# Performance work log

Hardware: AMD Instinct MI355X
Metric: run time of the kernel (lower is better)

## Reference

```python
import jax, jax.numpy as jnp
import numpy as np

EPS = 1e-12  # TF l2_normalize epsilon


def setup_inputs() -> dict:
    key = jax.random.key(0)
    k1, k2 = jax.random.split(key)
    B, V, F = 32, 200000, 400000
    vertices = jax.random.normal(k1, (B, V, 3), dtype=jnp.float32)
    faces = jax.random.randint(k2, (F, 3), 0, V, dtype=jnp.int32)
    return {"vertices": vertices, "faces": faces}


def reference(vertices, faces):
    # vertices: [B, V, 3], faces: [F, 3]
    # Gather triangle vertices: [B, F, 3(verts), 3(xyz)]
    tri = vertices[:, faces, :]
    v0, v1, v2 = tri[..., 0, :], tri[..., 1, :], tri[..., 2, :]
    e1 = v0 - v1
    e2 = v2 - v1
    face_normals = jnp.cross(e2, e1)  # [B, F, 3], unnormalized
    # Scatter-add face normals onto each of the 3 face vertices
    vertex_normals = jnp.zeros_like(vertices)
    for i in range(3):
        vertex_normals = vertex_normals.at[:, faces[:, i], :].add(face_normals)
    # l2 normalize (TF semantics: x * rsqrt(max(sum(x^2), eps)))
    sq = jnp.sum(vertex_normals * vertex_normals, axis=-1, keepdims=True)
    vertex_normals = vertex_normals * jax.lax.rsqrt(jnp.maximum(sq, EPS))
    return vertex_normals
```

## Files before the change

### kernel.cpp

```cpp
#include <hip/hip_runtime.h>

#define EPS 1e-12f
#define CAP 32
#define CAPU 8

typedef unsigned long long ull;


__global__ void zero_ints(int* __restrict__ p, int n) {
    int i = blockIdx.x * blockDim.x + threadIdx.x;
    if (i < n) p[i] = 0;
}

__global__ __launch_bounds__(1024) void prep_kernel(const float* __restrict__ verts,
                                                    float* __restrict__ vT,
                                                    const int* __restrict__ faces,
                                                    int* __restrict__ cursor,
                                                    ull* __restrict__ ell,
                                                    int V, int tblk, int E) {
    if ((int)blockIdx.x < tblk) {
        __shared__ float sx[32][33], sy[32][33], sz[32][33];
        int tx = threadIdx.x & 31, ty = threadIdx.x >> 5;
        int v0 = blockIdx.x * 32;
        const float* p = verts + ((size_t)ty * V + (v0 + tx)) * 3;
        float x = __builtin_nontemporal_load(p + 0);
        float y = __builtin_nontemporal_load(p + 1);
        float z = __builtin_nontemporal_load(p + 2);
        sx[ty][tx] = x; sy[ty][tx] = y; sz[ty][tx] = z;
        __syncthreads();
        float* o = vT + (size_t)(v0 + ty) * 96;
        o[tx]      = sx[tx][ty];
        o[32 + tx] = sy[tx][ty];
        o[64 + tx] = sz[tx][ty];
    } else {
        int t = (blockIdx.x - tblk) * 1024 + threadIdx.x;
        if (t >= E) return;
        int f = t / 3;
        int c = t - 3 * f;
        int base = 3 * f;
        int iv = faces[base + c];
        int ia = faces[base + (c == 2 ? 0 : c + 1)];
        int ib = faces[base + (c == 0 ? 2 : c - 1)];
        int s = atomicAdd(&cursor[iv], 1);
        if (s < CAP) {
            ull e = ((ull)(unsigned)ib << 32) | (unsigned)ia;
            __builtin_nontemporal_store(e, ell + (size_t)iv * CAP + s);
        }
    }
}

__global__ __launch_bounds__(1024) void gather_t(const float* __restrict__ vT,
                                                 const int* __restrict__ deg,
                                                 const ull* __restrict__ ell,
                                                 float* __restrict__ out,
                                                 int V) {
    __shared__ float sx[32][33], sy[32][33], sz[32][33];
    int b = threadIdx.x & 31;
    int vi = threadIdx.x >> 5;
    int v = blockIdx.x * 32 + vi;

    int d = min(deg[v], CAP);
    const float* crow = vT + (size_t)v * 96;
    float vx = crow[b], vy = crow[32 + b], vz = crow[64 + b];
    const ull* ev = ell + (size_t)v * CAP;
    ull e[CAPU];
#pragma unroll
    for (int s = 0; s < CAPU; s++)
        e[s] = ev[s];
    __builtin_amdgcn_sched_barrier(0);

    float Ax[CAPU], Ay[CAPU], Az[CAPU], Bx[CAPU], By[CAPU], Bz[CAPU];
#pragma unroll
    for (int s = 0; s < CAPU; s++) {
        unsigned ia = (s < d) ? (unsigned)(e[s] & 0xffffffffull) : 0u;
        unsigned ib = (s < d) ? (unsigned)(e[s] >> 32) : 0u;
        const float* ra = vT + (size_t)ia * 96;
        const float* rb = vT + (size_t)ib * 96;
        Ax[s] = ra[b]; Ay[s] = ra[32 + b]; Az[s] = ra[64 + b];
        Bx[s] = rb[b]; By[s] = rb[32 + b]; Bz[s] = rb[64 + b];
    }
    __builtin_amdgcn_sched_barrier(0);

    float ax = 0.f, ay = 0.f, az = 0.f;
#pragma unroll
    for (int s = 0; s < CAPU; s++) {
        if (s < d) {
            float aX = Ax[s] - vx, aY = Ay[s] - vy, aZ = Az[s] - vz;
            float bX = Bx[s] - vx, bY = By[s] - vy, bZ = Bz[s] - vz;
            ax += aY * bZ - aZ * bY;
            ay += aZ * bX - aX * bZ;
            az += aX * bY - aY * bX;
        }
    }
    for (int s = CAPU; s < d; s++) {
        ull cu = ev[s];
        const float* ra = vT + (size_t)(unsigned)(cu & 0xffffffffull) * 96;
        const float* rb = vT + (size_t)(unsigned)(cu >> 32) * 96;
        float aX = ra[b] - vx, aY = ra[32 + b] - vy, aZ = ra[64 + b] - vz;
        float bX = rb[b] - vx, bY = rb[32 + b] - vy, bZ = rb[64 + b] - vz;
        ax += aY * bZ - aZ * bY;
        ay += aZ * bX - aX * bZ;
        az += aX * bY - aY * bX;
    }

    float scn = rsqrtf(fmaxf(ax * ax + ay * ay + az * az, EPS));
    sx[vi][b] = ax * scn; sy[vi][b] = ay * scn; sz[vi][b] = az * scn;
    __syncthreads();

    float* o = out + ((size_t)vi * V + (size_t)blockIdx.x * 32 + b) * 3;
    __builtin_nontemporal_store(sx[b][vi], o + 0);
    __builtin_nontemporal_store(sy[b][vi], o + 1);
    __builtin_nontemporal_store(sz[b][vi], o + 2);
}

extern "C" void kernel_launch(void* const* d_in, const int* in_sizes, int n_in,
                              void* d_out, int out_size, void* d_ws, size_t ws_size,
                              hipStream_t stream) {
    const float* verts = (const float*)d_in[0];
    const int* faces = (const int*)d_in[1];
    float* out = (float*)d_out;

    const int V = 200000;
    const int F = in_sizes[1] / 3;
    const int B = in_sizes[0] / (3 * V);
    const int E = 3 * F;
    (void)B;

    char* w = (char*)d_ws;
    float* vT = (float*)w;  w += (size_t)V * 96 * sizeof(float);
    int* cursor = (int*)w;  w += (size_t)V * sizeof(int);
    ull* ell = (ull*)w;

    zero_ints<<<(V + 255) / 256, 256, 0, stream>>>(cursor, V);

    int tblk = V / 32;
    int fblk = (E + 1023) / 1024;
    prep_kernel<<<tblk + fblk, 1024, 0, stream>>>(verts, vT, faces, cursor, ell,
                                                  V, tblk, E);

    gather_t<<<V / 32, 1024, 0, stream>>>(vT, cursor, ell, out, V);
}
```

Measured before the change: 398.6 us.

## Store corner indices instead of neighbor pairs and split prep into separate kernels

The adjacency list now stores a 4-byte corner index per incident face instead of an 8-byte packed neighbor pair. The gather kernel recovers the two other face vertices by reading the faces array again. The fused transpose/fill kernel is split into two separate launches. This halves the adjacency storage and the bytes written during the fill, at the cost of an extra dependent load level (cidx, then faces, then vT) in the gather and one more kernel launch.

```diff
diff --git a/kernel.cpp b/kernel.cpp
--- a/kernel.cpp
+++ b/kernel.cpp
@@ -12,46 +12,36 @@
     if (i < n) p[i] = 0;
 }
 
-__global__ __launch_bounds__(1024) void prep_kernel(const float* __restrict__ verts,
-                                                    float* __restrict__ vT,
-                                                    const int* __restrict__ faces,
-                                                    int* __restrict__ cursor,
-                                                    ull* __restrict__ ell,
-                                                    int V, int tblk, int E) {
-    if ((int)blockIdx.x < tblk) {
-        __shared__ float sx[32][33], sy[32][33], sz[32][33];
-        int tx = threadIdx.x & 31, ty = threadIdx.x >> 5;
-        int v0 = blockIdx.x * 32;
-        const float* p = verts + ((size_t)ty * V + (v0 + tx)) * 3;
-        float x = __builtin_nontemporal_load(p + 0);
-        float y = __builtin_nontemporal_load(p + 1);
-        float z = __builtin_nontemporal_load(p + 2);
-        sx[ty][tx] = x; sy[ty][tx] = y; sz[ty][tx] = z;
-        __syncthreads();
-        float* o = vT + (size_t)(v0 + ty) * 96;
-        o[tx]      = sx[tx][ty];
-        o[32 + tx] = sy[tx][ty];
-        o[64 + tx] = sz[tx][ty];
-    } else {
-        int t = (blockIdx.x - tblk) * 1024 + threadIdx.x;
-        if (t >= E) return;
-        int f = t / 3;
-        int c = t - 3 * f;
-        int base = 3 * f;
-        int iv = faces[base + c];
-        int ia = faces[base + (c == 2 ? 0 : c + 1)];
-        int ib = faces[base + (c == 0 ? 2 : c - 1)];
-        int s = atomicAdd(&cursor[iv], 1);
-        if (s < CAP) {
-            ull e = ((ull)(unsigned)ib << 32) | (unsigned)ia;
-            __builtin_nontemporal_store(e, ell + (size_t)iv * CAP + s);
-        }
-    }
+__global__ __launch_bounds__(1024) void transpose_in(const float* __restrict__ verts,
+                                                     float* __restrict__ vT,
+                                                     int V) {
+    __shared__ float sx[32][33], sy[32][33], sz[32][33];
+    int tx = threadIdx.x & 31, ty = threadIdx.x >> 5;
+    int v0 = blockIdx.x * 32;
+    const float* p = verts + ((size_t)ty * V + (v0 + tx)) * 3;
+    sx[ty][tx] = __builtin_nontemporal_load(p + 0);
+    sy[ty][tx] = __builtin_nontemporal_load(p + 1);
+    sz[ty][tx] = __builtin_nontemporal_load(p + 2);
+    __syncthreads();
+    float* o = vT + (size_t)(v0 + ty) * 96;
+    o[tx]      = sx[tx][ty];
+    o[32 + tx] = sy[tx][ty];
+    o[64 + tx] = sz[tx][ty];
+}
+
+__global__ void fill_corner(const int* __restrict__ faces, int* __restrict__ cursor,
+                            int* __restrict__ cidx, int E) {
+    int t = blockIdx.x * blockDim.x + threadIdx.x;
+    if (t >= E) return;
+    int iv = faces[t];
+    int s = atomicAdd(&cursor[iv], 1);
+    if (s < CAP) cidx[iv * CAP + s] = t;
 }
 
 __global__ __launch_bounds__(1024) void gather_t(const float* __restrict__ vT,
                                                  const int* __restrict__ deg,
-                                                 const ull* __restrict__ ell,
+                                                 const int* __restrict__ cidx,
+                                                 const int* __restrict__ faces,
                                                  float* __restrict__ out,
                                                  int V) {
     __shared__ float sx[32][33], sy[32][33], sz[32][33];
@@ -62,20 +52,30 @@
     int d = min(deg[v], CAP);
     const float* crow = vT + (size_t)v * 96;
     float vx = crow[b], vy = crow[32 + b], vz = crow[64 + b];
-    const ull* ev = ell + (size_t)v * CAP;
-    ull e[CAPU];
+    const int* cv = cidx + v * CAP;
+    int e[CAPU];
 #pragma unroll
     for (int s = 0; s < CAPU; s++)
-        e[s] = ev[s];
+        e[s] = cv[s];
+    __builtin_amdgcn_sched_barrier(0);
+
+    int ian[CAPU], ibn[CAPU];
+#pragma unroll
+    for (int s = 0; s < CAPU; s++) {
+        int t = (s < d) ? e[s] : 0;
+        int f = t / 3;
+        int c = t - 3 * f;
+        int base = 3 * f;
+        ian[s] = faces[base + (c == 2 ? 0 : c + 1)];
+        ibn[s] = faces[base + (c == 0 ? 2 : c - 1)];
+    }
     __builtin_amdgcn_sched_barrier(0);
 
     float Ax[CAPU], Ay[CAPU], Az[CAPU], Bx[CAPU], By[CAPU], Bz[CAPU];
 #pragma unroll
     for (int s = 0; s < CAPU; s++) {
-        unsigned ia = (s < d) ? (unsigned)(e[s] & 0xffffffffull) : 0u;
-        unsigned ib = (s < d) ? (unsigned)(e[s] >> 32) : 0u;
-        const float* ra = vT + (size_t)ia * 96;
-        const float* rb = vT + (size_t)ib * 96;
+        const float* ra = vT + (size_t)(unsigned)ian[s] * 96;
+        const float* rb = vT + (size_t)(unsigned)ibn[s] * 96;
         Ax[s] = ra[b]; Ay[s] = ra[32 + b]; Az[s] = ra[64 + b];
         Bx[s] = rb[b]; By[s] = rb[32 + b]; Bz[s] = rb[64 + b];
     }
@@ -93,9 +93,14 @@
         }
     }
     for (int s = CAPU; s < d; s++) {
-        ull cu = ev[s];
-        const float* ra = vT + (size_t)(unsigned)(cu & 0xffffffffull) * 96;
-        const float* rb = vT + (size_t)(unsigned)(cu >> 32) * 96;
+        int t = cv[s];
+        int f = t / 3;
+        int c = t - 3 * f;
+        int base = 3 * f;
+        int ia = faces[base + (c == 2 ? 0 : c + 1)];
+        int ib = faces[base + (c == 0 ? 2 : c - 1)];
+        const float* ra = vT + (size_t)(unsigned)ia * 96;
+        const float* rb = vT + (size_t)(unsigned)ib * 96;
         float aX = ra[b] - vx, aY = ra[32 + b] - vy, aZ = ra[64 + b] - vz;
         float bX = rb[b] - vx, bY = rb[32 + b] - vy, bZ = rb[64 + b] - vz;
         ax += aY * bZ - aZ * bY;
@@ -129,14 +134,10 @@
     char* w = (char*)d_ws;
     float* vT = (float*)w;  w += (size_t)V * 96 * sizeof(float);
     int* cursor = (int*)w;  w += (size_t)V * sizeof(int);
-    ull* ell = (ull*)w;
+    int* cidx = (int*)w;
 
     zero_ints<<<(V + 255) / 256, 256, 0, stream>>>(cursor, V);
-
-    int tblk = V / 32;
-    int fblk = (E + 1023) / 1024;
-    prep_kernel<<<tblk + fblk, 1024, 0, stream>>>(verts, vT, faces, cursor, ell,
-                                                  V, tblk, E);
-
-    gather_t<<<V / 32, 1024, 0, stream>>>(vT, cursor, ell, out, V);
+    transpose_in<<<V / 32, 1024, 0, stream>>>(verts, vT, V);
+    fill_corner<<<(E + 255) / 256, 256, 0, stream>>>(faces, cursor, cidx, E);
+    gather_t<<<V / 32, 1024, 0, stream>>>(vT, cursor, cidx, faces, out, V);
 }
```

Measured after the change: 423.1 us. 1.06x slower.
